# Performance work log

Hardware: AMD Instinct MI355X
Metric: run time of the kernel (lower is better)

Reference implementation:

```python
import jax, jax.numpy as jnp
import numpy as np

B, H, S, D = 2, 16, 2048, 64


def setup_inputs() -> dict:
    key = jax.random.key(0)
    kq, kk, kv = jax.random.split(key, 3)
    Q = jax.random.normal(kq, (B, H, S, D), dtype=jnp.float32)
    K = jax.random.normal(kk, (B, H, S, D), dtype=jnp.float32)
    V = jax.random.normal(kv, (B, H, S, D), dtype=jnp.float32)
    # causal mask: True = masked out (matches torch masked_fill_ semantics)
    causal = ~jnp.tril(jnp.ones((S, S), dtype=bool))
    mask = jnp.broadcast_to(causal, (B, H, S, S))
    return {"Q": Q, "K": K, "V": V, "mask": mask}


def reference(Q, K, V, mask):
    d_q = Q.shape[-1]
    scale = 1.0 / np.sqrt(d_q).astype(np.float32)
    # scores: (B, H, S, S)
    scores = jnp.einsum('bhqd,bhkd->bhqk', Q, K) * scale
    scores = jnp.where(mask, jnp.float32(-1e9), scores)
    attention = jax.nn.softmax(scores, axis=-1)
    context = jnp.einsum('bhqk,bhkd->bhqd', attention, V)
    return (context, attention)
```

## Files before the change

kernel.cpp:

```cpp
#include <hip/hip_runtime.h>
#include <hip/hip_bf16.h>


constexpr int SEQ = 2048;
constexpr int HD  = 64;
constexpr int NHEADS = 32;
constexpr int QT  = 64;
constexpr int NT  = SEQ / QT;

typedef __bf16 bf16x8 __attribute__((ext_vector_type(8)));
typedef unsigned short u16x8 __attribute__((ext_vector_type(8)));
typedef unsigned short u16x4 __attribute__((ext_vector_type(4)));
typedef float f32x4 __attribute__((ext_vector_type(4)));
typedef unsigned short us;

__device__ __forceinline__ us f2bf(float x) {
  unsigned u = __builtin_bit_cast(unsigned, x);
  return (us)((u + 0x7fffu + ((u >> 16) & 1u)) >> 16);
}
__device__ __forceinline__ float bf2f(us b) {
  return __builtin_bit_cast(float, (unsigned)b << 16);
}

#define GLOAD_LDS(gp, lp)                                                        \
  __builtin_amdgcn_global_load_lds(                                             \
      (const __attribute__((address_space(1))) void*)(gp),                      \
      (__attribute__((address_space(3))) void*)(lp), 16, 0, 0)

__device__ __forceinline__ void stage8k(const us* img, us* lds, int w, int l) {
  const char* g = (const char*)img + w * 2048 + l * 16;
  char* s = (char*)lds + w * 2048;
  GLOAD_LDS(g, s);
  GLOAD_LDS(g + 1024, s + 1024);
}

__global__ void prep_kernel(const float* __restrict__ Qg,
                            const float* __restrict__ Kg,
                            const float* __restrict__ Vg,
                            us* __restrict__ ws) {
  const int tile = blockIdx.x & (NT - 1);
  const int bh   = blockIdx.x >> 5;
  const int t = threadIdx.x;
  const size_t tOff = ((size_t)bh * SEQ + (size_t)tile * QT) * HD;
  us* Qi = ws + ((size_t)bh * NT + tile) * 4096;
  us* Ki = Qi + (size_t)NHEADS * NT * 4096;
  us* Vi = Ki + (size_t)NHEADS * NT * 4096;

  #pragma unroll
  for (int g0 = 0; g0 < 2; ++g0) {
    const int g = t + 256 * g0;
    const int r = g >> 3, c8 = g & 7;
    const int cp = (8 * c8) ^ ((r & 7) << 3);
    const float* qs = Qg + tOff + (size_t)r * HD + cp;
    const float* ks = Kg + tOff + (size_t)r * HD + cp;
    u16x8 q, k;
    #pragma unroll
    for (int j = 0; j < 8; ++j) { q[j] = f2bf(qs[j]); k[j] = f2bf(ks[j]); }
    *(u16x8*)(Qi + 8 * g) = q;
    *(u16x8*)(Ki + 8 * g) = k;
  }
  #pragma unroll
  for (int g0 = 0; g0 < 2; ++g0) {
    const int g = t + 256 * g0;
    const int d = g >> 3, k8 = g & 7;
    const int kp = (8 * k8) ^ ((d & 7) << 3);
    const float* vs = Vg + tOff + d;
    u16x8 v;
    #pragma unroll
    for (int j = 0; j < 8; ++j) v[j] = f2bf(vs[(size_t)(kp + j) * HD]);
    *(u16x8*)(Vi + 8 * g) = v;
  }
}

__launch_bounds__(256, 3)
__global__ void attn_main(const us* __restrict__ ws, float* __restrict__ out) {
  const int fb = blockIdx.x;
  const int bh = fb & (NHEADS - 1);
  const int pi = fb >> 5;
  const int t  = threadIdx.x;
  const int l  = t & 63;
  const int w  = t >> 6;
  const int l16 = l & 15;
  const int lg  = l >> 4;

  __shared__ __align__(16) us Ks[2][4096];
  __shared__ __align__(16) us Vs[2][4096];
  __shared__ __align__(16) us Ps[4][1024];

  const us* Qi = ws + (size_t)bh * NT * 4096;
  const us* Ki = Qi + (size_t)NHEADS * NT * 4096;
  const us* Vi = Ki + (size_t)NHEADS * NT * 4096;

  float* ctx = out + (size_t)bh * SEQ * HD;
  float* att = out + (size_t)NHEADS * SEQ * HD + (size_t)bh * SEQ * SEQ;

  const float KC = 0.18033688011112042f;

  for (int half = 0; half < 2; ++half) {
    const int qt = half ? (NT - 1 - pi) : pi;
    const int qbase = qt * QT;
    const int qg = qbase + w * 16 + l16;

    stage8k(Ki, Ks[0], w, l);
    bf16x8 aq[2];
    {
      const int qr = w * 16 + l16;
      #pragma unroll
      for (int ks = 0; ks < 2; ++ks) {
        const int idx = (qr * 64 + ks * 32 + lg * 8) ^ ((qr & 7) << 3);
        aq[ks] = __builtin_bit_cast(bf16x8, *(const u16x8*)(&Qi[(size_t)qt * 4096 + idx]));
      }
    }
    {
      const int zc0 = (qt + 1) * QT;
      const int nz4 = (SEQ - zc0) >> 2;
      for (int rr = 0; rr < QT; ++rr) {
        float* rowp = att + (size_t)(qbase + rr) * SEQ + zc0;
        for (int c = t; c < nz4; c += 256)
          __builtin_nontemporal_store((f32x4){0.f, 0.f, 0.f, 0.f}, (f32x4*)(rowp + 4 * c));
      }
    }
    __syncthreads();

    float rsum = 0.f;
    {
      int cur = 0;
      for (int kt = 0; kt <= qt; ++kt) {
        if (kt < qt) stage8k(Ki + (size_t)(kt + 1) * 4096, Ks[cur ^ 1], w, l);
        const us* krb = Ks[cur];
        const int kb = kt * QT;
        #pragma unroll
        for (int ct = 0; ct < 4; ++ct) {
          f32x4 acc = {0.f, 0.f, 0.f, 0.f};
          #pragma unroll
          for (int ks = 0; ks < 2; ++ks) {
            const int kr = ct * 16 + l16;
            const int idx = (kr * 64 + ks * 32 + lg * 8) ^ ((kr & 7) << 3);
            bf16x8 bk = __builtin_bit_cast(bf16x8, *(const u16x8*)(&krb[idx]));
            acc = __builtin_amdgcn_mfma_f32_16x16x32_bf16(bk, aq[ks], acc, 0, 0, 0);
          }
          const int kg0 = kb + ct * 16 + lg * 4;
          #pragma unroll
          for (int rr = 0; rr < 4; ++rr) {
            float e = __builtin_amdgcn_exp2f(acc[rr] * KC);
            rsum += (kg0 + rr <= qg) ? e : 0.f;
          }
        }
        __syncthreads();
        cur ^= 1;
      }
    }
    stage8k(Ki, Ks[0], w, l);
    stage8k(Vi, Vs[0], w, l);
    rsum += __shfl_xor(rsum, 16);
    rsum += __shfl_xor(rsum, 32);
    const float inv = 1.f / rsum;
    __syncthreads();

    f32x4 oacc[4];
    #pragma unroll
    for (int ct = 0; ct < 4; ++ct) oacc[ct] = (f32x4){0.f, 0.f, 0.f, 0.f};

    {
      int cur = 0;
      for (int kt = 0; kt <= qt; ++kt) {
        if (kt < qt) {
          stage8k(Ki + (size_t)(kt + 1) * 4096, Ks[cur ^ 1], w, l);
          stage8k(Vi + (size_t)(kt + 1) * 4096, Vs[cur ^ 1], w, l);
        }
        __builtin_amdgcn_sched_barrier(0);
        const us* krb = Ks[cur];
        const us* vrb = Vs[cur];
        const int kb = kt * QT;

        #pragma unroll
        for (int ct = 0; ct < 4; ++ct) {
          f32x4 acc = {0.f, 0.f, 0.f, 0.f};
          #pragma unroll
          for (int ks = 0; ks < 2; ++ks) {
            const int kr = ct * 16 + l16;
            const int idx = (kr * 64 + ks * 32 + lg * 8) ^ ((kr & 7) << 3);
            bf16x8 bk = __builtin_bit_cast(bf16x8, *(const u16x8*)(&krb[idx]));
            acc = __builtin_amdgcn_mfma_f32_16x16x32_bf16(bk, aq[ks], acc, 0, 0, 0);
          }
          const int kg0 = kb + ct * 16 + lg * 4;
          u16x4 pb;
          #pragma unroll
          for (int rr = 0; rr < 4; ++rr) {
            float e = __builtin_amdgcn_exp2f(acc[rr] * KC) * inv;
            pb[rr] = f2bf((kg0 + rr <= qg) ? e : 0.f);
          }
          const int pidx = (l16 * 64 + ct * 16 + lg * 4) ^ ((l16 & 7) << 3);
          *(u16x4*)(&Ps[w][pidx]) = pb;
        }

        #pragma unroll
        for (int j = 0; j < 4; ++j) {
          const int rloc = lg + 4 * j;
          const int idx = (rloc * 64 + 4 * l16) ^ ((rloc & 7) << 3);
          u16x4 p4 = *(const u16x4*)(&Ps[w][idx]);
          f32x4 pv = { bf2f(p4[0]), bf2f(p4[1]), bf2f(p4[2]), bf2f(p4[3]) };
          __builtin_nontemporal_store(pv,
              (f32x4*)(att + (size_t)(qbase + w * 16 + rloc) * SEQ + kb + 4 * l16));
        }

        bf16x8 pa[2];
        #pragma unroll
        for (int ks = 0; ks < 2; ++ks) {
          const int pidx = (l16 * 64 + ks * 32 + lg * 8) ^ ((l16 & 7) << 3);
          pa[ks] = __builtin_bit_cast(bf16x8, *(const u16x8*)(&Ps[w][pidx]));
        }
        #pragma unroll
        for (int ct = 0; ct < 4; ++ct) {
          #pragma unroll
          for (int ks = 0; ks < 2; ++ks) {
            const int dr = ct * 16 + l16;
            const int vidx = (dr * 64 + ks * 32 + lg * 8) ^ ((dr & 7) << 3);
            bf16x8 av = __builtin_bit_cast(bf16x8, *(const u16x8*)(&vrb[vidx]));
            oacc[ct] = __builtin_amdgcn_mfma_f32_16x16x32_bf16(av, pa[ks], oacc[ct], 0, 0, 0);
          }
        }

        if (kt < qt) {
          asm volatile("s_waitcnt vmcnt(4) lgkmcnt(0)" ::: "memory");
        } else {
          asm volatile("s_waitcnt lgkmcnt(0)" ::: "memory");
        }
        __builtin_amdgcn_s_barrier();
        __builtin_amdgcn_sched_barrier(0);
        cur ^= 1;
      }
    }

    #pragma unroll
    for (int ct = 0; ct < 4; ++ct)
      __builtin_nontemporal_store(oacc[ct],
          (f32x4*)(ctx + (size_t)qg * HD + ct * 16 + lg * 4));
  }
}

__launch_bounds__(256, 2)
__global__ void attn_fallback(const float* __restrict__ Qg,
                              const float* __restrict__ Kg,
                              const float* __restrict__ Vg,
                              float* __restrict__ out) {
  const int fb = blockIdx.x;
  const int bh = fb & (NHEADS - 1);
  const int pi = fb >> 5;
  const int t  = threadIdx.x;
  const int l  = t & 63;
  const int w  = t >> 6;
  const int l16 = l & 15;
  const int lg  = l >> 4;

  __shared__ __align__(16) us Qs[QT * HD];
  __shared__ __align__(16) us Ks[QT * HD];
  __shared__ __align__(16) us Vs[QT * HD];
  __shared__ __align__(16) us Ps[4][16 * QT];

  const size_t hoff = (size_t)bh * SEQ * HD;
  const float* Qh = Qg + hoff;
  const float* Kh = Kg + hoff;
  const float* Vh = Vg + hoff;
  float* ctx = out + hoff;
  float* att = out + (size_t)NHEADS * SEQ * HD + (size_t)bh * SEQ * SEQ;

  auto load_tile = [&](const float* src, f32x4 (&reg)[4]) {
    #pragma unroll
    for (int j = 0; j < 4; ++j) {
      const int f = t + 256 * j;
      reg[j] = *(const f32x4*)(src + (size_t)(f >> 4) * HD + 4 * (f & 15));
    }
  };
  auto write_k = [&](const f32x4 (&reg)[4], us* dst) {
    #pragma unroll
    for (int j = 0; j < 4; ++j) {
      const int f = t + 256 * j;
      const int rr = f >> 4, c4 = f & 15;
      const int idx = (rr * 64 + 4 * c4) ^ ((rr & 7) << 3);
      u16x4 b = { f2bf(reg[j].x), f2bf(reg[j].y), f2bf(reg[j].z), f2bf(reg[j].w) };
      *(u16x4*)(&dst[idx]) = b;
    }
  };
  auto write_vv = [&](const f32x4 (&reg)[4], us* dst) {
    #pragma unroll
    for (int j = 0; j < 4; ++j) {
      const int f = t + 256 * j;
      const int rr = f >> 4, c4 = f & 15;
      const int idx = (rr * 64 + 4 * c4) ^ (((rr >> 3) & 3) << 4);
      u16x4 b = { f2bf(reg[j].x), f2bf(reg[j].y), f2bf(reg[j].z), f2bf(reg[j].w) };
      *(u16x4*)(&dst[idx]) = b;
    }
  };

  const float sc = 0.125f;

  for (int half = 0; half < 2; ++half) {
    const int qt = half ? (NT - 1 - pi) : pi;
    const int qbase = qt * QT;
    const int qg = qbase + w * 16 + l16;

    __syncthreads();
    {
      const int zc0 = (qt + 1) * QT;
      const int nz4 = (SEQ - zc0) >> 2;
      for (int rr = 0; rr < QT; ++rr) {
        float* rowp = att + (size_t)(qbase + rr) * SEQ + zc0;
        for (int c = t; c < nz4; c += 256)
          __builtin_nontemporal_store((f32x4){0.f, 0.f, 0.f, 0.f}, (f32x4*)(rowp + 4 * c));
      }
    }
    {
      f32x4 qreg[4];
      load_tile(Qh + (size_t)qbase * HD, qreg);
      write_k(qreg, Qs);
    }
    __syncthreads();

    bf16x8 aq[2];
    #pragma unroll
    for (int ks = 0; ks < 2; ++ks) {
      const int qr = w * 16 + l16;
      const int idx = (qr * 64 + ks * 32 + lg * 8) ^ ((qr & 7) << 3);
      aq[ks] = __builtin_bit_cast(bf16x8, *(const u16x8*)(&Qs[idx]));
    }

    float rsum = 0.f;
    {
      f32x4 kreg[4];
      load_tile(Kh, kreg);
      write_k(kreg, Ks);
      __syncthreads();
      for (int kt = 0; kt <= qt; ++kt) {
        if (kt < qt) load_tile(Kh + (size_t)(kt + 1) * QT * HD, kreg);
        const int kb = kt * QT;
        #pragma unroll
        for (int ct = 0; ct < 4; ++ct) {
          f32x4 acc = {0.f, 0.f, 0.f, 0.f};
          #pragma unroll
          for (int ks = 0; ks < 2; ++ks) {
            const int kr = ct * 16 + l16;
            const int idx = (kr * 64 + ks * 32 + lg * 8) ^ ((kr & 7) << 3);
            bf16x8 bk = __builtin_bit_cast(bf16x8, *(const u16x8*)(&Ks[idx]));
            acc = __builtin_amdgcn_mfma_f32_16x16x32_bf16(bk, aq[ks], acc, 0, 0, 0);
          }
          const int kg0 = kb + ct * 16 + lg * 4;
          #pragma unroll
          for (int rr = 0; rr < 4; ++rr) {
            float e = __expf(acc[rr] * sc);
            rsum += (kg0 + rr <= qg) ? e : 0.f;
          }
        }
        __syncthreads();
        if (kt < qt) write_k(kreg, Ks);
        __syncthreads();
      }
    }
    rsum += __shfl_xor(rsum, 16);
    rsum += __shfl_xor(rsum, 32);
    const float inv = 1.f / rsum;

    f32x4 oacc[4];
    #pragma unroll
    for (int ct = 0; ct < 4; ++ct) oacc[ct] = (f32x4){0.f, 0.f, 0.f, 0.f};

    {
      f32x4 kreg[4], vreg[4];
      load_tile(Kh, kreg);
      load_tile(Vh, vreg);
      write_k(kreg, Ks);
      write_vv(vreg, Vs);
      __syncthreads();
      for (int kt = 0; kt <= qt; ++kt) {
        if (kt < qt) {
          load_tile(Kh + (size_t)(kt + 1) * QT * HD, kreg);
          load_tile(Vh + (size_t)(kt + 1) * QT * HD, vreg);
        }
        const int kb = kt * QT;
        #pragma unroll
        for (int ct = 0; ct < 4; ++ct) {
          f32x4 acc = {0.f, 0.f, 0.f, 0.f};
          #pragma unroll
          for (int ks = 0; ks < 2; ++ks) {
            const int kr = ct * 16 + l16;
            const int idx = (kr * 64 + ks * 32 + lg * 8) ^ ((kr & 7) << 3);
            bf16x8 bk = __builtin_bit_cast(bf16x8, *(const u16x8*)(&Ks[idx]));
            acc = __builtin_amdgcn_mfma_f32_16x16x32_bf16(bk, aq[ks], acc, 0, 0, 0);
          }
          const int kg0 = kb + ct * 16 + lg * 4;
          u16x4 pb;
          #pragma unroll
          for (int rr = 0; rr < 4; ++rr) {
            float e = __expf(acc[rr] * sc) * inv;
            pb[rr] = f2bf((kg0 + rr <= qg) ? e : 0.f);
          }
          const int pidx = (l16 * 64 + ct * 16 + lg * 4) ^ ((l16 & 7) << 3);
          *(u16x4*)(&Ps[w][pidx]) = pb;
        }
        #pragma unroll
        for (int ct = 0; ct < 4; ++ct) {
          #pragma unroll
          for (int ks = 0; ks < 2; ++ks) {
            const int key0 = ks * 32 + lg * 8;
            const int pidx = (l16 * 64 + key0) ^ ((l16 & 7) << 3);
            bf16x8 pa = __builtin_bit_cast(bf16x8, *(const u16x8*)(&Ps[w][pidx]));
            bf16x8 av;
            const int dcol = ct * 16 + l16;
            const int xorv = ((key0 >> 3) & 3) << 4;
            #pragma unroll
            for (int j = 0; j < 8; ++j)
              av[j] = __builtin_bit_cast(__bf16, Vs[((key0 + j) * 64 + dcol) ^ xorv]);
            oacc[ct] = __builtin_amdgcn_mfma_f32_16x16x32_bf16(av, pa, oacc[ct], 0, 0, 0);
          }
        }
        __syncthreads();
        #pragma unroll
        for (int j = 0; j < 4; ++j) {
          const int f = t + 256 * j;
          const int rr = f >> 4, c4 = f & 15;
          const int ww = rr >> 4, qr = rr & 15;
          const int idx = (qr * 64 + 4 * c4) ^ ((qr & 7) << 3);
          u16x4 pb = *(const u16x4*)(&Ps[ww][idx]);
          f32x4 pv = { bf2f(pb[0]), bf2f(pb[1]), bf2f(pb[2]), bf2f(pb[3]) };
          __builtin_nontemporal_store(pv,
              (f32x4*)(att + (size_t)(qbase + rr) * SEQ + kb + 4 * c4));
        }
        if (kt < qt) {
          write_k(kreg, Ks);
          write_vv(vreg, Vs);
        }
        __syncthreads();
      }
    }
    #pragma unroll
    for (int ct = 0; ct < 4; ++ct)
      *(f32x4*)(ctx + (size_t)qg * HD + ct * 16 + lg * 4) = oacc[ct];
  }
}

extern "C" void kernel_launch(void* const* d_in, const int* in_sizes, int n_in,
                              void* d_out, int out_size, void* d_ws, size_t ws_size,
                              hipStream_t stream) {
  const float* Q = (const float*)d_in[0];
  const float* K = (const float*)d_in[1];
  const float* V = (const float*)d_in[2];
  float* out = (float*)d_out;
  const size_t NEED = (size_t)3 * NHEADS * NT * 4096 * sizeof(us);
  if (ws_size >= NEED && d_ws != nullptr) {
    us* wsp = (us*)d_ws;
    prep_kernel<<<dim3(NHEADS * NT), dim3(256), 0, stream>>>(Q, K, V, wsp);
    attn_main<<<dim3(NT / 2 * NHEADS), dim3(256), 0, stream>>>(wsp, out);
  } else {
    attn_fallback<<<dim3(NT / 2 * NHEADS), dim3(256), 0, stream>>>(Q, K, V, out);
  }
}
```

Before: 145.4 us.

## Split attention work into 32-row query tiles with 128-thread blocks

The main attention kernel now assigns 32 query rows per block with 2 waves (128 threads) instead of 64 rows with 4 waves, doubling the grid to 1024 blocks. K/V tiles remain 64 keys and are staged by all 128 threads with four 16-byte LDS loads each. The hand-tuned waitcnt/s_barrier and sched_barrier hints are replaced with a plain __syncthreads. The aim is finer load balance and more blocks across CUs, at the cost of reloading each K/V tile for twice as many blocks and weaker load/compute overlap.

```diff
diff --git a/kernel.cpp b/kernel.cpp
--- a/kernel.cpp
+++ b/kernel.cpp
@@ -5,8 +5,8 @@
 constexpr int SEQ = 2048;
 constexpr int HD  = 64;
 constexpr int NHEADS = 32;
-constexpr int QT  = 64;
-constexpr int NT  = SEQ / QT;
+constexpr int NTK = 32;
+constexpr int NTQ = 64;
 
 typedef __bf16 bf16x8 __attribute__((ext_vector_type(8)));
 typedef unsigned short u16x8 __attribute__((ext_vector_type(8)));
@@ -27,24 +27,26 @@
       (const __attribute__((address_space(1))) void*)(gp),                      \
       (__attribute__((address_space(3))) void*)(lp), 16, 0, 0)
 
-__device__ __forceinline__ void stage8k(const us* img, us* lds, int w, int l) {
-  const char* g = (const char*)img + w * 2048 + l * 16;
-  char* s = (char*)lds + w * 2048;
+__device__ __forceinline__ void stage8k_128(const us* img, us* lds, int t) {
+  const char* g = (const char*)img + t * 16;
+  char* s = (char*)lds + t * 16;
   GLOAD_LDS(g, s);
-  GLOAD_LDS(g + 1024, s + 1024);
+  GLOAD_LDS(g + 2048, s + 2048);
+  GLOAD_LDS(g + 4096, s + 4096);
+  GLOAD_LDS(g + 6144, s + 6144);
 }
 
 __global__ void prep_kernel(const float* __restrict__ Qg,
                             const float* __restrict__ Kg,
                             const float* __restrict__ Vg,
                             us* __restrict__ ws) {
-  const int tile = blockIdx.x & (NT - 1);
+  const int tile = blockIdx.x & (NTK - 1);
   const int bh   = blockIdx.x >> 5;
   const int t = threadIdx.x;
-  const size_t tOff = ((size_t)bh * SEQ + (size_t)tile * QT) * HD;
-  us* Qi = ws + ((size_t)bh * NT + tile) * 4096;
-  us* Ki = Qi + (size_t)NHEADS * NT * 4096;
-  us* Vi = Ki + (size_t)NHEADS * NT * 4096;
+  const size_t tOff = ((size_t)bh * SEQ + (size_t)tile * 64) * HD;
+  us* Qi = ws + ((size_t)bh * NTK + tile) * 4096;
+  us* Ki = Qi + (size_t)NHEADS * NTK * 4096;
+  us* Vi = Ki + (size_t)NHEADS * NTK * 4096;
 
   #pragma unroll
   for (int g0 = 0; g0 < 2; ++g0) {
@@ -72,7 +74,7 @@
   }
 }
 
-__launch_bounds__(256, 3)
+__launch_bounds__(128, 2)
 __global__ void attn_main(const us* __restrict__ ws, float* __restrict__ out) {
   const int fb = blockIdx.x;
   const int bh = fb & (NHEADS - 1);
@@ -85,11 +87,11 @@
 
   __shared__ __align__(16) us Ks[2][4096];
   __shared__ __align__(16) us Vs[2][4096];
-  __shared__ __align__(16) us Ps[4][1024];
-
-  const us* Qi = ws + (size_t)bh * NT * 4096;
-  const us* Ki = Qi + (size_t)NHEADS * NT * 4096;
-  const us* Vi = Ki + (size_t)NHEADS * NT * 4096;
+  __shared__ __align__(16) us Ps[2][1024];
+
+  const us* Qi = ws + (size_t)bh * NTK * 4096;
+  const us* Ki = Qi + (size_t)NHEADS * NTK * 4096;
+  const us* Vi = Ki + (size_t)NHEADS * NTK * 4096;
 
   float* ctx = out + (size_t)bh * SEQ * HD;
   float* att = out + (size_t)NHEADS * SEQ * HD + (size_t)bh * SEQ * SEQ;
@@ -97,26 +99,29 @@
   const float KC = 0.18033688011112042f;
 
   for (int half = 0; half < 2; ++half) {
-    const int qt = half ? (NT - 1 - pi) : pi;
-    const int qbase = qt * QT;
+    const int qt = half ? (NTQ - 1 - pi) : pi;
+    const int KT = qt >> 1;
+    const int qbase = qt * 32;
     const int qg = qbase + w * 16 + l16;
 
-    stage8k(Ki, Ks[0], w, l);
     bf16x8 aq[2];
     {
-      const int qr = w * 16 + l16;
+      const int qr = (qt & 1) * 32 + w * 16 + l16;
+      const us* Qimg = Qi + (size_t)(qt >> 1) * 4096;
       #pragma unroll
       for (int ks = 0; ks < 2; ++ks) {
         const int idx = (qr * 64 + ks * 32 + lg * 8) ^ ((qr & 7) << 3);
-        aq[ks] = __builtin_bit_cast(bf16x8, *(const u16x8*)(&Qi[(size_t)qt * 4096 + idx]));
-      }
-    }
-    {
-      const int zc0 = (qt + 1) * QT;
+        aq[ks] = __builtin_bit_cast(bf16x8, *(const u16x8*)(&Qimg[idx]));
+      }
+    }
+
+    stage8k_128(Ki, Ks[0], t);
+    {
+      const int zc0 = (KT + 1) * 64;
       const int nz4 = (SEQ - zc0) >> 2;
-      for (int rr = 0; rr < QT; ++rr) {
+      for (int rr = 0; rr < 32; ++rr) {
         float* rowp = att + (size_t)(qbase + rr) * SEQ + zc0;
-        for (int c = t; c < nz4; c += 256)
+        for (int c = t; c < nz4; c += 128)
           __builtin_nontemporal_store((f32x4){0.f, 0.f, 0.f, 0.f}, (f32x4*)(rowp + 4 * c));
       }
     }
@@ -125,10 +130,10 @@
     float rsum = 0.f;
     {
       int cur = 0;
-      for (int kt = 0; kt <= qt; ++kt) {
-        if (kt < qt) stage8k(Ki + (size_t)(kt + 1) * 4096, Ks[cur ^ 1], w, l);
+      for (int kt = 0; kt <= KT; ++kt) {
+        if (kt < KT) stage8k_128(Ki + (size_t)(kt + 1) * 4096, Ks[cur ^ 1], t);
         const us* krb = Ks[cur];
-        const int kb = kt * QT;
+        const int kb = kt * 64;
         #pragma unroll
         for (int ct = 0; ct < 4; ++ct) {
           f32x4 acc = {0.f, 0.f, 0.f, 0.f};
@@ -150,8 +155,8 @@
         cur ^= 1;
       }
     }
-    stage8k(Ki, Ks[0], w, l);
-    stage8k(Vi, Vs[0], w, l);
+    stage8k_128(Ki, Ks[0], t);
+    stage8k_128(Vi, Vs[0], t);
     rsum += __shfl_xor(rsum, 16);
     rsum += __shfl_xor(rsum, 32);
     const float inv = 1.f / rsum;
@@ -163,15 +168,14 @@
 
     {
       int cur = 0;
-      for (int kt = 0; kt <= qt; ++kt) {
-        if (kt < qt) {
-          stage8k(Ki + (size_t)(kt + 1) * 4096, Ks[cur ^ 1], w, l);
-          stage8k(Vi + (size_t)(kt + 1) * 4096, Vs[cur ^ 1], w, l);
-        }
-        __builtin_amdgcn_sched_barrier(0);
+      for (int kt = 0; kt <= KT; ++kt) {
+        if (kt < KT) {
+          stage8k_128(Ki + (size_t)(kt + 1) * 4096, Ks[cur ^ 1], t);
+          stage8k_128(Vi + (size_t)(kt + 1) * 4096, Vs[cur ^ 1], t);
+        }
         const us* krb = Ks[cur];
         const us* vrb = Vs[cur];
-        const int kb = kt * QT;
+        const int kb = kt * 64;
 
         #pragma unroll
         for (int ct = 0; ct < 4; ++ct) {
@@ -221,13 +225,7 @@
           }
         }
 
-        if (kt < qt) {
-          asm volatile("s_waitcnt vmcnt(4) lgkmcnt(0)" ::: "memory");
-        } else {
-          asm volatile("s_waitcnt lgkmcnt(0)" ::: "memory");
-        }
-        __builtin_amdgcn_s_barrier();
-        __builtin_amdgcn_sched_barrier(0);
+        __syncthreads();
         cur ^= 1;
       }
     }
@@ -253,10 +251,10 @@
   const int l16 = l & 15;
   const int lg  = l >> 4;
 
-  __shared__ __align__(16) us Qs[QT * HD];
-  __shared__ __align__(16) us Ks[QT * HD];
-  __shared__ __align__(16) us Vs[QT * HD];
-  __shared__ __align__(16) us Ps[4][16 * QT];
+  __shared__ __align__(16) us Qs[64 * HD];
+  __shared__ __align__(16) us Ks[64 * HD];
+  __shared__ __align__(16) us Vs[64 * HD];
+  __shared__ __align__(16) us Ps[4][16 * 64];
 
   const size_t hoff = (size_t)bh * SEQ * HD;
   const float* Qh = Qg + hoff;
@@ -296,15 +294,15 @@
   const float sc = 0.125f;
 
   for (int half = 0; half < 2; ++half) {
-    const int qt = half ? (NT - 1 - pi) : pi;
-    const int qbase = qt * QT;
+    const int qt = half ? (31 - pi) : pi;
+    const int qbase = qt * 64;
     const int qg = qbase + w * 16 + l16;
 
     __syncthreads();
     {
-      const int zc0 = (qt + 1) * QT;
+      const int zc0 = (qt + 1) * 64;
       const int nz4 = (SEQ - zc0) >> 2;
-      for (int rr = 0; rr < QT; ++rr) {
+      for (int rr = 0; rr < 64; ++rr) {
         float* rowp = att + (size_t)(qbase + rr) * SEQ + zc0;
         for (int c = t; c < nz4; c += 256)
           __builtin_nontemporal_store((f32x4){0.f, 0.f, 0.f, 0.f}, (f32x4*)(rowp + 4 * c));
@@ -332,8 +330,8 @@
       write_k(kreg, Ks);
       __syncthreads();
       for (int kt = 0; kt <= qt; ++kt) {
-        if (kt < qt) load_tile(Kh + (size_t)(kt + 1) * QT * HD, kreg);
-        const int kb = kt * QT;
+        if (kt < qt) load_tile(Kh + (size_t)(kt + 1) * 64 * HD, kreg);
+        const int kb = kt * 64;
         #pragma unroll
         for (int ct = 0; ct < 4; ++ct) {
           f32x4 acc = {0.f, 0.f, 0.f, 0.f};
@@ -373,10 +371,10 @@
       __syncthreads();
       for (int kt = 0; kt <= qt; ++kt) {
         if (kt < qt) {
-          load_tile(Kh + (size_t)(kt + 1) * QT * HD, kreg);
-          load_tile(Vh + (size_t)(kt + 1) * QT * HD, vreg);
-        }
-        const int kb = kt * QT;
+          load_tile(Kh + (size_t)(kt + 1) * 64 * HD, kreg);
+          load_tile(Vh + (size_t)(kt + 1) * 64 * HD, vreg);
+        }
+        const int kb = kt * 64;
         #pragma unroll
         for (int ct = 0; ct < 4; ++ct) {
           f32x4 acc = {0.f, 0.f, 0.f, 0.f};
@@ -445,12 +443,12 @@
   const float* K = (const float*)d_in[1];
   const float* V = (const float*)d_in[2];
   float* out = (float*)d_out;
-  const size_t NEED = (size_t)3 * NHEADS * NT * 4096 * sizeof(us);
+  const size_t NEED = (size_t)3 * NHEADS * NTK * 4096 * sizeof(us);
   if (ws_size >= NEED && d_ws != nullptr) {
     us* wsp = (us*)d_ws;
-    prep_kernel<<<dim3(NHEADS * NT), dim3(256), 0, stream>>>(Q, K, V, wsp);
-    attn_main<<<dim3(NT / 2 * NHEADS), dim3(256), 0, stream>>>(wsp, out);
+    prep_kernel<<<dim3(NHEADS * NTK), dim3(256), 0, stream>>>(Q, K, V, wsp);
+    attn_main<<<dim3(NTQ / 2 * NHEADS), dim3(128), 0, stream>>>(wsp, out);
   } else {
-    attn_fallback<<<dim3(NT / 2 * NHEADS), dim3(256), 0, stream>>>(Q, K, V, out);
+    attn_fallback<<<dim3(16 * NHEADS), dim3(256), 0, stream>>>(Q, K, V, out);
   }
 }
```

Measured after the change: 159.1 us. 9.4% more time.
